# Kernel optimization log

Measured on AMD Instinct MI355X. Metric: run time of the kernel, lower is better.

The kernel has to match this reference:

```python
import jax, jax.numpy as jnp
import numpy as np

D_MODEL = 512
D_FF = 2048
VOCAB = 32000
B, N = 2, 384
EPS = 1e-6


def positional_encoding(n, d):
    pos = np.arange(n)[:, None].astype(np.float64)
    i = np.arange(d)[None, :]
    ang = pos / np.power(10000.0, (2 * (i // 2)) / np.float32(d))
    ang[:, 0::2] = np.sin(ang[:, 0::2])
    ang[:, 1::2] = np.cos(ang[:, 1::2])
    return jnp.asarray(ang, dtype=jnp.float32)  # [n, d]


def layer_norm(x, gamma, beta):
    mu = jnp.mean(x, axis=-1, keepdims=True)
    var = jnp.mean(jnp.square(x - mu), axis=-1, keepdims=True)
    return (x - mu) / jnp.sqrt(var + EPS) * gamma + beta


def setup_inputs() -> dict:
    key = jax.random.key(0)
    ks = jax.random.split(key, 12)
    s = 0.02
    return {
        "tokens": jax.random.randint(ks[0], (B, N), 0, VOCAB, dtype=jnp.int32),
        "emb": jax.random.normal(ks[1], (VOCAB, D_MODEL), jnp.float32) * s,
        "Wq": jax.random.normal(ks[2], (D_MODEL, D_MODEL), jnp.float32) * s,
        "bq": jnp.zeros((D_MODEL,), jnp.float32),
        "Wk": jax.random.normal(ks[3], (D_MODEL, D_MODEL), jnp.float32) * s,
        "bk": jnp.zeros((D_MODEL,), jnp.float32),
        "Wv": jax.random.normal(ks[4], (D_MODEL, D_MODEL), jnp.float32) * s,
        "bv": jnp.zeros((D_MODEL,), jnp.float32),
        "attn_scale": jax.random.normal(ks[5], (D_MODEL,), jnp.float32) * 0.05,
        "Wo": jax.random.normal(ks[6], (D_MODEL, D_MODEL), jnp.float32) * s,
        "bo": jnp.zeros((D_MODEL,), jnp.float32),
        "g1": jnp.ones((D_MODEL,), jnp.float32),
        "beta1": jnp.zeros((D_MODEL,), jnp.float32),
        "W1": jax.random.normal(ks[7], (D_MODEL, D_FF), jnp.float32) * s,
        "bf1": jnp.zeros((D_FF,), jnp.float32),
        "W2": jax.random.normal(ks[8], (D_FF, D_MODEL), jnp.float32) * s,
        "bf2": jnp.zeros((D_MODEL,), jnp.float32),
        "g2": jnp.ones((D_MODEL,), jnp.float32),
        "beta2": jnp.zeros((D_MODEL,), jnp.float32),
    }


def reference(tokens, emb, Wq, bq, Wk, bk, Wv, bv, attn_scale, Wo, bo,
              g1, beta1, W1, bf1, W2, bf2, g2, beta2):
    # Embedding + scaled positional encoding
    x = emb[tokens] * jnp.sqrt(jnp.float32(D_MODEL))  # [B, N, D]
    x = x + positional_encoding(N, D_MODEL)[None, :, :]

    # Additive (Bahdanau) self-attention
    q = x @ Wq + bq
    k = x @ Wk + bk  # note: original swaps key/value Dense layers; math-equivalent
    v = x @ Wv + bv
    # scores[b,i,j] = sum_d scale[d] * tanh(q[b,i,d] + k[b,j,d])  -> [B,N,N]
    scores = jnp.einsum("d,bijd->bij", attn_scale,
                        jnp.tanh(q[:, :, None, :] + k[:, None, :, :]))
    weights = jax.nn.softmax(scores, axis=-1)
    attn = jnp.einsum("bij,bjd->bid", weights, v)
    attn = attn @ Wo + bo
    x = layer_norm(x + attn, g1, beta1)

    # Feedforward + residual + LayerNorm
    h = jax.nn.relu(x @ W1 + bf1)
    y = h @ W2 + bf2
    return layer_norm(x + y, g2, beta2)
```

## Files before the change

kernel.cpp:

```cpp
#include <hip/hip_runtime.h>
#include <hip/hip_bf16.h>
#include <math.h>

#define D_MODEL 512
#define D_FF    2048
#define NBATCH  2
#define NSEQ    384
#define NROWS   (NBATCH * NSEQ)
#define LN_EPS  1e-6f

typedef __attribute__((ext_vector_type(8))) short short8;
typedef __attribute__((ext_vector_type(4))) short short4v;
typedef __attribute__((ext_vector_type(4))) float f32x4;
typedef __hip_bfloat16 bf16;

static __device__ __forceinline__ short bfb(float x) {
    bf16 h = __float2bfloat16(x);
    return *reinterpret_cast<short*>(&h);
}

__global__ __launch_bounds__(256) void wt_all_kernel(
    const float* __restrict__ Wq, const float* __restrict__ Wk,
    const float* __restrict__ Wv, const float* __restrict__ Wo,
    const float* __restrict__ W1, const float* __restrict__ W2,
    bf16* __restrict__ wqt, bf16* __restrict__ wkt, bf16* __restrict__ wvt,
    bf16* __restrict__ wot, bf16* __restrict__ w1t, bf16* __restrict__ w2t)
{
    int t = blockIdx.x;
    const float* W; bf16* Wt; int K, N, bx, by;
    if (t < 1024) {
        int w = t >> 8, rem = t & 255;
        W  = (w == 0) ? Wq  : (w == 1) ? Wk  : (w == 2) ? Wv  : Wo;
        Wt = (w == 0) ? wqt : (w == 1) ? wkt : (w == 2) ? wvt : wot;
        K = 512; N = 512; bx = rem & 15; by = rem >> 4;
    } else if (t < 2048) {
        int rem = t - 1024;
        W = W1; Wt = w1t; K = 512; N = 2048; bx = rem & 63; by = rem >> 6;
    } else {
        int rem = t - 2048;
        W = W2; Wt = w2t; K = 2048; N = 512; bx = rem & 15; by = rem >> 4;
    }

    __shared__ float tile[32][33];
    int tx = threadIdx.x & 31, ty = threadIdx.x >> 5;
    #pragma unroll
    for (int r = ty; r < 32; r += 8)
        tile[r][tx] = W[(size_t)(by * 32 + r) * N + bx * 32 + tx];
    __syncthreads();
    #pragma unroll
    for (int r = ty; r < 32; r += 8)
        Wt[(size_t)(bx * 32 + r) * K + by * 32 + tx] = __float2bfloat16(tile[tx][r]);
}

__global__ __launch_bounds__(256) void embed_pe_kernel(
    const int* __restrict__ tokens, const float* __restrict__ emb,
    float* __restrict__ x, bf16* __restrict__ xb)
{
    int row = blockIdx.x;
    int n   = row % NSEQ;
    int tok = tokens[row];
    const float sqrtD = 22.627416997969522f;
    for (int d = threadIdx.x; d < D_MODEL; d += 256) {
        float e = emb[tok * D_MODEL + d] * sqrtD;
        int   i2   = d & ~1;
        float expo = (float)i2 / (float)D_MODEL;
        float ang  = (float)n * powf(10000.0f, -expo);
        float pe   = (d & 1) ? cosf(ang) : sinf(ang);
        float val  = e + pe;
        x [(size_t)row * D_MODEL + d] = val;
        xb[(size_t)row * D_MODEL + d] = __float2bfloat16(val);
    }
}

__global__ __launch_bounds__(256) void qkv_mfma_kernel(
    const bf16* __restrict__ A,
    const bf16* __restrict__ wqt, const bf16* __restrict__ wkt, const bf16* __restrict__ wvt,
    const float* __restrict__ bq, const float* __restrict__ bk, const float* __restrict__ bv,
    float* __restrict__ aexp, float* __restrict__ bexp, bf16* __restrict__ vT)
{
    int z = blockIdx.z;
    const bf16*  Wt   = (z == 0) ? wqt : (z == 1) ? wkt : wvt;
    const float* bias = (z == 0) ? bq  : (z == 1) ? bk  : bv;

    int lane = threadIdx.x & 63, wid = threadIdx.x >> 6;
    int rowBase = blockIdx.y * 32 + (wid >> 1) * 16;
    int colBase = blockIdx.x * 64 + (wid & 1) * 32;

    const bf16* Ap  = A  + (size_t)(rowBase + (lane & 15)) * D_MODEL + ((lane >> 4) << 3);
    const bf16* Bp0 = Wt + (size_t)(colBase + (lane & 15)) * D_MODEL + ((lane >> 4) << 3);
    const bf16* Bp1 = Bp0 + (size_t)16 * D_MODEL;

    f32x4 acc0 = {0.f, 0.f, 0.f, 0.f};
    f32x4 acc1 = {0.f, 0.f, 0.f, 0.f};

    #pragma unroll 4
    for (int k0 = 0; k0 < D_MODEL; k0 += 32) {
        short8 a  = *reinterpret_cast<const short8*>(Ap  + k0);
        short8 b0 = *reinterpret_cast<const short8*>(Bp0 + k0);
        short8 b1 = *reinterpret_cast<const short8*>(Bp1 + k0);
        acc0 = __builtin_amdgcn_mfma_f32_16x16x32_bf16(a, b0, acc0, 0, 0, 0);
        acc1 = __builtin_amdgcn_mfma_f32_16x16x32_bf16(a, b1, acc1, 0, 0, 0);
    }

    int crow = rowBase + ((lane >> 4) << 2);
    int ccol = colBase + (lane & 15);

    if (z < 2) {
        float* C = (z == 0) ? aexp : bexp;
        #pragma unroll
        for (int r = 0; r < 4; ++r) {
            int row = crow + r;
            #pragma unroll
            for (int j = 0; j < 2; ++j) {
                int col = ccol + j * 16;
                float val = (j == 0 ? acc0[r] : acc1[r]) + bias[col];
                C[(size_t)row * D_MODEL + col] = __expf(2.0f * val);
            }
        }
    } else {
        int bb = crow / NSEQ;
        int jr = crow - bb * NSEQ;
        #pragma unroll
        for (int j = 0; j < 2; ++j) {
            int col = ccol + j * 16;
            short4v pk;
            #pragma unroll
            for (int r = 0; r < 4; ++r)
                pk[r] = bfb((j == 0 ? acc0[r] : acc1[r]) + bias[col]);
            size_t idx = ((size_t)bb * D_MODEL + col) * NSEQ + jr;
            *reinterpret_cast<short4v*>((short*)vT + idx) = pk;
        }
    }
}

__global__ __launch_bounds__(512) void score_softmax_kernel(
    const float* __restrict__ aexp, const float* __restrict__ bexp,
    const float* __restrict__ scale, bf16* __restrict__ P)
{
    int row0 = blockIdx.x * 2;
    int b    = row0 / NSEQ;
    int tid  = threadIdx.x;
    int lane = tid & 63, wid = tid >> 6;

    __shared__ float a0s[D_MODEL], a1s[D_MODEL], s2s[D_MODEL];
    __shared__ float sc[2][NSEQ];
    __shared__ float red[8];

    a0s[tid] = aexp[(size_t)row0 * D_MODEL + tid];
    a1s[tid] = aexp[(size_t)(row0 + 1) * D_MODEL + tid];
    s2s[tid] = -2.0f * scale[tid];
    __syncthreads();

    float a0[8], a1[8], sv[8];
    #pragma unroll
    for (int u = 0; u < 8; ++u) {
        a0[u] = a0s[lane * 8 + u];
        a1[u] = a1s[lane * 8 + u];
        sv[u] = s2s[lane * 8 + u];
    }

    const float* kb = bexp + (size_t)b * NSEQ * D_MODEL + lane * 8;
    for (int j = wid; j < NSEQ; j += 8) {
        const float4* kp = (const float4*)(kb + (size_t)j * D_MODEL);
        float4 b0 = kp[0], b1 = kp[1];
        float bb[8] = {b0.x, b0.y, b0.z, b0.w, b1.x, b1.y, b1.z, b1.w};
        float t0 = 0.0f, t1 = 0.0f;
        #pragma unroll
        for (int u = 0; u < 8; ++u) {
            float r0 = __builtin_amdgcn_rcpf(fmaf(a0[u], bb[u], 1.0f));
            float r1 = __builtin_amdgcn_rcpf(fmaf(a1[u], bb[u], 1.0f));
            t0 = fmaf(sv[u], r0, t0);
            t1 = fmaf(sv[u], r1, t1);
        }
        #pragma unroll
        for (int off = 32; off; off >>= 1) {
            t0 += __shfl_xor(t0, off, 64);
            t1 += __shfl_xor(t1, off, 64);
        }
        if (lane == 0) { sc[0][j] = t0; sc[1][j] = t1; }
    }
    __syncthreads();

    #pragma unroll
    for (int r = 0; r < 2; ++r) {
        float e = (tid < NSEQ) ? __expf(sc[r][tid]) : 0.0f;
        float s = e;
        #pragma unroll
        for (int off = 32; off; off >>= 1) s += __shfl_xor(s, off, 64);
        if (lane == 0) red[wid] = s;
        __syncthreads();
        if (tid == 0) {
            float t = 0.0f;
            #pragma unroll
            for (int w = 0; w < 8; ++w) t += red[w];
            red[0] = t;
        }
        __syncthreads();
        float inv = 1.0f / red[0];
        if (tid < NSEQ)
            P[(size_t)(row0 + r) * NSEQ + tid] = __float2bfloat16(e * inv);
        __syncthreads();
    }
}

__global__ __launch_bounds__(256) void pv_mfma_kernel(
    const bf16* __restrict__ P, const bf16* __restrict__ vT,
    bf16* __restrict__ attnb)
{
    int z = blockIdx.z;
    int lane = threadIdx.x & 63, wid = threadIdx.x >> 6;
    int rowBase = blockIdx.y * 32 + (wid >> 1) * 16;
    int colBase = blockIdx.x * 64 + (wid & 1) * 32;

    const bf16* Ap  = P  + ((size_t)z * NSEQ + rowBase + (lane & 15)) * NSEQ + ((lane >> 4) << 3);
    const bf16* Bp0 = vT + ((size_t)z * D_MODEL + colBase + (lane & 15)) * NSEQ + ((lane >> 4) << 3);
    const bf16* Bp1 = Bp0 + (size_t)16 * NSEQ;

    f32x4 acc0 = {0.f, 0.f, 0.f, 0.f};
    f32x4 acc1 = {0.f, 0.f, 0.f, 0.f};

    #pragma unroll 4
    for (int k0 = 0; k0 < NSEQ; k0 += 32) {
        short8 a  = *reinterpret_cast<const short8*>(Ap  + k0);
        short8 b0 = *reinterpret_cast<const short8*>(Bp0 + k0);
        short8 b1 = *reinterpret_cast<const short8*>(Bp1 + k0);
        acc0 = __builtin_amdgcn_mfma_f32_16x16x32_bf16(a, b0, acc0, 0, 0, 0);
        acc1 = __builtin_amdgcn_mfma_f32_16x16x32_bf16(a, b1, acc1, 0, 0, 0);
    }

    int crow = rowBase + ((lane >> 4) << 2);
    int ccol = colBase + (lane & 15);
    #pragma unroll
    for (int r = 0; r < 4; ++r)
        #pragma unroll
        for (int j = 0; j < 2; ++j)
            attnb[((size_t)z * NSEQ + crow + r) * D_MODEL + ccol + j * 16] =
                __float2bfloat16(j == 0 ? acc0[r] : acc1[r]);
}

__global__ __launch_bounds__(256) void mfma_gemm_kernel(
    const bf16* __restrict__ A, const bf16* __restrict__ Wt,
    const float* __restrict__ bias, const float* __restrict__ resid,
    float* __restrict__ Cf, bf16* __restrict__ Cb,
    int K, int N, int relu)
{
    int lane = threadIdx.x & 63, wid = threadIdx.x >> 6;
    int rowBase = blockIdx.y * 32 + (wid >> 1) * 16;
    int colBase = blockIdx.x * 64 + (wid & 1) * 32;

    const bf16* Ap  = A  + (size_t)(rowBase + (lane & 15)) * K + ((lane >> 4) << 3);
    const bf16* Bp0 = Wt + (size_t)(colBase + (lane & 15)) * K + ((lane >> 4) << 3);
    const bf16* Bp1 = Bp0 + (size_t)16 * K;

    f32x4 acc0 = {0.f, 0.f, 0.f, 0.f};
    f32x4 acc1 = {0.f, 0.f, 0.f, 0.f};

    #pragma unroll 4
    for (int k0 = 0; k0 < K; k0 += 32) {
        short8 a  = *reinterpret_cast<const short8*>(Ap  + k0);
        short8 b0 = *reinterpret_cast<const short8*>(Bp0 + k0);
        short8 b1 = *reinterpret_cast<const short8*>(Bp1 + k0);
        acc0 = __builtin_amdgcn_mfma_f32_16x16x32_bf16(a, b0, acc0, 0, 0, 0);
        acc1 = __builtin_amdgcn_mfma_f32_16x16x32_bf16(a, b1, acc1, 0, 0, 0);
    }

    int crow = rowBase + ((lane >> 4) << 2);
    int ccol = colBase + (lane & 15);
    #pragma unroll
    for (int r = 0; r < 4; ++r) {
        int row = crow + r;
        #pragma unroll
        for (int j = 0; j < 2; ++j) {
            int col = ccol + j * 16;
            float val = (j == 0 ? acc0[r] : acc1[r]) + bias[col];
            if (resid) val += resid[(size_t)row * N + col];
            if (relu)  val = fmaxf(val, 0.0f);
            if (Cf) Cf[(size_t)row * N + col] = val;
            if (Cb) Cb[(size_t)row * N + col] = __float2bfloat16(val);
        }
    }
}

__global__ __launch_bounds__(256) void ln_kernel(
    const float* __restrict__ in, const float* __restrict__ gamma,
    const float* __restrict__ beta, float* __restrict__ out,
    bf16* __restrict__ outb)
{
    int row = blockIdx.x;
    int tid = threadIdx.x;
    int lane = tid & 63, wid = tid >> 6;
    __shared__ float red[4];

    float v0 = in[(size_t)row * D_MODEL + tid];
    float v1 = in[(size_t)row * D_MODEL + tid + 256];

    float s = v0 + v1;
    #pragma unroll
    for (int off = 32; off; off >>= 1) s += __shfl_xor(s, off, 64);
    if (lane == 0) red[wid] = s;
    __syncthreads();
    if (tid == 0) red[0] = red[0] + red[1] + red[2] + red[3];
    __syncthreads();
    float mu = red[0] * (1.0f / D_MODEL);
    __syncthreads();

    float d0 = v0 - mu, d1 = v1 - mu;
    float s2 = d0 * d0 + d1 * d1;
    #pragma unroll
    for (int off = 32; off; off >>= 1) s2 += __shfl_xor(s2, off, 64);
    if (lane == 0) red[wid] = s2;
    __syncthreads();
    if (tid == 0) red[0] = red[0] + red[1] + red[2] + red[3];
    __syncthreads();
    float var = red[0] * (1.0f / D_MODEL);
    float inv = rsqrtf(var + LN_EPS);

    float o0 = d0 * inv * gamma[tid] + beta[tid];
    float o1 = d1 * inv * gamma[tid + 256] + beta[tid + 256];
    out[(size_t)row * D_MODEL + tid]       = o0;
    out[(size_t)row * D_MODEL + tid + 256] = o1;
    if (outb) {
        outb[(size_t)row * D_MODEL + tid]       = __float2bfloat16(o0);
        outb[(size_t)row * D_MODEL + tid + 256] = __float2bfloat16(o1);
    }
}

extern "C" void kernel_launch(void* const* d_in, const int* in_sizes, int n_in,
                              void* d_out, int out_size, void* d_ws, size_t ws_size,
                              hipStream_t stream)
{
    const int*   tokens = (const int*)  d_in[0];
    const float* emb    = (const float*)d_in[1];
    const float* Wq     = (const float*)d_in[2];
    const float* bq     = (const float*)d_in[3];
    const float* Wk     = (const float*)d_in[4];
    const float* bk     = (const float*)d_in[5];
    const float* Wv     = (const float*)d_in[6];
    const float* bv     = (const float*)d_in[7];
    const float* ascale = (const float*)d_in[8];
    const float* Wo     = (const float*)d_in[9];
    const float* bo     = (const float*)d_in[10];
    const float* g1     = (const float*)d_in[11];
    const float* beta1  = (const float*)d_in[12];
    const float* W1     = (const float*)d_in[13];
    const float* bf1    = (const float*)d_in[14];
    const float* W2     = (const float*)d_in[15];
    const float* bf2    = (const float*)d_in[16];
    const float* g2     = (const float*)d_in[17];
    const float* beta2  = (const float*)d_in[18];

    float* out = (float*)d_out;
    float* ws  = (float*)d_ws;

    const size_t SZ = (size_t)NROWS * D_MODEL;

    float* x0   = ws;
    float* aexp = ws + 1 * SZ;
    float* bexp = ws + 2 * SZ;
    float* t1 = aexp;
    float* x1 = bexp;
    float* y  = x0;

    bf16* x0b   = (bf16*)(ws + 3 * SZ);
    bf16* attnb = x0b + SZ;
    bf16* x1b   = attnb + SZ;
    bf16* hb    = x1b + SZ;
    bf16* Pb    = hb + (size_t)NROWS * D_FF;
    bf16* vTb   = Pb + (size_t)NBATCH * NSEQ * NSEQ;
    bf16* wqt   = vTb + (size_t)NBATCH * D_MODEL * NSEQ;
    bf16* wkt   = wqt + (size_t)D_MODEL * D_MODEL;
    bf16* wvt   = wkt + (size_t)D_MODEL * D_MODEL;
    bf16* wot   = wvt + (size_t)D_MODEL * D_MODEL;
    bf16* w1t   = wot + (size_t)D_MODEL * D_MODEL;
    bf16* w2t   = w1t + (size_t)D_MODEL * D_FF;

    wt_all_kernel<<<3072, 256, 0, stream>>>(Wq, Wk, Wv, Wo, W1, W2,
                                            wqt, wkt, wvt, wot, w1t, w2t);

    embed_pe_kernel<<<NROWS, 256, 0, stream>>>(tokens, emb, x0, x0b);

    qkv_mfma_kernel<<<dim3(D_MODEL / 64, NROWS / 32, 3), 256, 0, stream>>>(
        x0b, wqt, wkt, wvt, bq, bk, bv, aexp, bexp, vTb);

    score_softmax_kernel<<<NROWS / 2, 512, 0, stream>>>(aexp, bexp, ascale, Pb);

    pv_mfma_kernel<<<dim3(D_MODEL / 64, NSEQ / 32, NBATCH), 256, 0, stream>>>(
        Pb, vTb, attnb);

    mfma_gemm_kernel<<<dim3(D_MODEL / 64, NROWS / 32), 256, 0, stream>>>(
        attnb, wot, bo, x0, t1, nullptr, D_MODEL, D_MODEL, 0);

    ln_kernel<<<NROWS, 256, 0, stream>>>(t1, g1, beta1, x1, x1b);

    mfma_gemm_kernel<<<dim3(D_FF / 64, NROWS / 32), 256, 0, stream>>>(
        x1b, w1t, bf1, nullptr, nullptr, hb, D_MODEL, D_FF, 1);

    mfma_gemm_kernel<<<dim3(D_MODEL / 64, NROWS / 32), 256, 0, stream>>>(
        hb, w2t, bf2, x1, y, nullptr, D_FF, D_MODEL, 0);

    ln_kernel<<<NROWS, 256, 0, stream>>>(y, g2, beta2, out, nullptr);
}
```

Measured before the change: 138.4 us.

## Split score kernel across halves and defer softmax normalization into PV epilogue

The score kernel now runs on a 2D grid with each block handling half the key positions, mapping lanes to (key, d-chunk) pairs and loading query/scale vectors directly from global memory instead of staging in shared memory. It writes unnormalized exponentials and per-half partial sums, and the PV GEMM divides by the combined sum in its epilogue. This aims to raise parallelism and remove the in-kernel softmax barriers. It adds a small partial-sum buffer and keeps the unnormalized exp values in bf16, with no max subtraction.

```diff
diff --git a/kernel.cpp b/kernel.cpp
--- a/kernel.cpp
+++ b/kernel.cpp
@@ -133,86 +133,102 @@
     }
 }
 
-__global__ __launch_bounds__(512) void score_softmax_kernel(
+__global__ __launch_bounds__(512) void score_kernel(
     const float* __restrict__ aexp, const float* __restrict__ bexp,
-    const float* __restrict__ scale, bf16* __restrict__ P)
-{
-    int row0 = blockIdx.x * 2;
+    const float* __restrict__ scale, bf16* __restrict__ E,
+    float* __restrict__ Sp)
+{
+    int ip   = blockIdx.x;
+    int half = blockIdx.y;
+    int row0 = ip * 2;
     int b    = row0 / NSEQ;
     int tid  = threadIdx.x;
     int lane = tid & 63, wid = tid >> 6;
-
-    __shared__ float a0s[D_MODEL], a1s[D_MODEL], s2s[D_MODEL];
-    __shared__ float sc[2][NSEQ];
-    __shared__ float red[8];
-
-    a0s[tid] = aexp[(size_t)row0 * D_MODEL + tid];
-    a1s[tid] = aexp[(size_t)(row0 + 1) * D_MODEL + tid];
-    s2s[tid] = -2.0f * scale[tid];
-    __syncthreads();
-
-    float a0[8], a1[8], sv[8];
-    #pragma unroll
-    for (int u = 0; u < 8; ++u) {
-        a0[u] = a0s[lane * 8 + u];
-        a1[u] = a1s[lane * 8 + u];
-        sv[u] = s2s[lane * 8 + u];
-    }
-
-    const float* kb = bexp + (size_t)b * NSEQ * D_MODEL + lane * 8;
-    for (int j = wid; j < NSEQ; j += 8) {
-        const float4* kp = (const float4*)(kb + (size_t)j * D_MODEL);
-        float4 b0 = kp[0], b1 = kp[1];
-        float bb[8] = {b0.x, b0.y, b0.z, b0.w, b1.x, b1.y, b1.z, b1.w};
-        float t0 = 0.0f, t1 = 0.0f;
-        #pragma unroll
-        for (int u = 0; u < 8; ++u) {
-            float r0 = __builtin_amdgcn_rcpf(fmaf(a0[u], bb[u], 1.0f));
-            float r1 = __builtin_amdgcn_rcpf(fmaf(a1[u], bb[u], 1.0f));
-            t0 = fmaf(sv[u], r0, t0);
-            t1 = fmaf(sv[u], r1, t1);
-        }
-        #pragma unroll
-        for (int off = 32; off; off >>= 1) {
+    int jj = lane & 7, dd = lane >> 3;
+
+    const float* a0p = aexp + (size_t)row0 * D_MODEL;
+    const float* a1p = a0p + D_MODEL;
+    const float* bb  = bexp + (size_t)b * NSEQ * D_MODEL;
+
+    int jbase = half * 192 + wid * 8 + jj;
+
+    float acc[3][2] = {};
+
+    #pragma unroll
+    for (int chunk = 0; chunk < 8; ++chunk) {
+        int doff = chunk * 64 + dd * 8;
+        float4 a0A = *(const float4*)(a0p + doff);
+        float4 a0B = *(const float4*)(a0p + doff + 4);
+        float4 a1A = *(const float4*)(a1p + doff);
+        float4 a1B = *(const float4*)(a1p + doff + 4);
+        float4 sA  = *(const float4*)(scale + doff);
+        float4 sB  = *(const float4*)(scale + doff + 4);
+        float a0[8] = {a0A.x,a0A.y,a0A.z,a0A.w,a0B.x,a0B.y,a0B.z,a0B.w};
+        float a1[8] = {a1A.x,a1A.y,a1A.z,a1A.w,a1B.x,a1B.y,a1B.z,a1B.w};
+        float sv[8] = {sA.x,sA.y,sA.z,sA.w,sB.x,sB.y,sB.z,sB.w};
+
+        #pragma unroll
+        for (int o = 0; o < 3; ++o) {
+            const float* bp = bb + (size_t)(jbase + o * 64) * D_MODEL + doff;
+            float4 b0 = *(const float4*)(bp);
+            float4 b1 = *(const float4*)(bp + 4);
+            float bv8[8] = {b0.x,b0.y,b0.z,b0.w,b1.x,b1.y,b1.z,b1.w};
+            float t0 = acc[o][0], t1 = acc[o][1];
+            #pragma unroll
+            for (int u = 0; u < 8; ++u) {
+                float r0 = __builtin_amdgcn_rcpf(fmaf(a0[u], bv8[u], 1.0f));
+                float r1 = __builtin_amdgcn_rcpf(fmaf(a1[u], bv8[u], 1.0f));
+                t0 = fmaf(sv[u], r0, t0);
+                t1 = fmaf(sv[u], r1, t1);
+            }
+            acc[o][0] = t0; acc[o][1] = t1;
+        }
+    }
+
+    __shared__ float sred[8][2];
+    float es0 = 0.0f, es1 = 0.0f;
+    #pragma unroll
+    for (int o = 0; o < 3; ++o) {
+        int j = jbase + o * 64;
+        float t0 = acc[o][0], t1 = acc[o][1];
+        #pragma unroll
+        for (int off = 8; off < 64; off <<= 1) {
             t0 += __shfl_xor(t0, off, 64);
             t1 += __shfl_xor(t1, off, 64);
         }
-        if (lane == 0) { sc[0][j] = t0; sc[1][j] = t1; }
-    }
-    __syncthreads();
-
-    #pragma unroll
-    for (int r = 0; r < 2; ++r) {
-        float e = (tid < NSEQ) ? __expf(sc[r][tid]) : 0.0f;
-        float s = e;
-        #pragma unroll
-        for (int off = 32; off; off >>= 1) s += __shfl_xor(s, off, 64);
-        if (lane == 0) red[wid] = s;
-        __syncthreads();
-        if (tid == 0) {
-            float t = 0.0f;
-            #pragma unroll
-            for (int w = 0; w < 8; ++w) t += red[w];
-            red[0] = t;
-        }
-        __syncthreads();
-        float inv = 1.0f / red[0];
-        if (tid < NSEQ)
-            P[(size_t)(row0 + r) * NSEQ + tid] = __float2bfloat16(e * inv);
-        __syncthreads();
+        float e0 = __expf(-2.0f * t0);
+        float e1 = __expf(-2.0f * t1);
+        if (dd == 0) {
+            E[(size_t)row0 * NSEQ + j]       = __float2bfloat16(e0);
+            E[(size_t)(row0+1) * NSEQ + j]   = __float2bfloat16(e1);
+        }
+        es0 += e0; es1 += e1;
+    }
+    #pragma unroll
+    for (int off = 1; off < 64; off <<= 1) {
+        es0 += __shfl_xor(es0, off, 64);
+        es1 += __shfl_xor(es1, off, 64);
+    }
+    if (lane == 0) { sred[wid][0] = es0 * 0.125f; sred[wid][1] = es1 * 0.125f; }
+    __syncthreads();
+    if (tid < 2) {
+        float s = 0.0f;
+        #pragma unroll
+        for (int w = 0; w < 8; ++w) s += sred[w][tid];
+        Sp[(size_t)(row0 + tid) * 2 + half] = s;
     }
 }
 
 __global__ __launch_bounds__(256) void pv_mfma_kernel(
-    const bf16* __restrict__ P, const bf16* __restrict__ vT,
-    bf16* __restrict__ attnb)
+    const bf16* __restrict__ E, const bf16* __restrict__ vT,
+    const float* __restrict__ Sp, bf16* __restrict__ attnb)
 {
     int z = blockIdx.z;
     int lane = threadIdx.x & 63, wid = threadIdx.x >> 6;
     int rowBase = blockIdx.y * 32 + (wid >> 1) * 16;
     int colBase = blockIdx.x * 64 + (wid & 1) * 32;
 
-    const bf16* Ap  = P  + ((size_t)z * NSEQ + rowBase + (lane & 15)) * NSEQ + ((lane >> 4) << 3);
+    const bf16* Ap  = E  + ((size_t)z * NSEQ + rowBase + (lane & 15)) * NSEQ + ((lane >> 4) << 3);
     const bf16* Bp0 = vT + ((size_t)z * D_MODEL + colBase + (lane & 15)) * NSEQ + ((lane >> 4) << 3);
     const bf16* Bp1 = Bp0 + (size_t)16 * NSEQ;
 
@@ -231,11 +247,14 @@
     int crow = rowBase + ((lane >> 4) << 2);
     int ccol = colBase + (lane & 15);
     #pragma unroll
-    for (int r = 0; r < 4; ++r)
+    for (int r = 0; r < 4; ++r) {
+        int grow = z * NSEQ + crow + r;
+        float Sinv = 1.0f / (Sp[(size_t)grow * 2] + Sp[(size_t)grow * 2 + 1]);
         #pragma unroll
         for (int j = 0; j < 2; ++j)
-            attnb[((size_t)z * NSEQ + crow + r) * D_MODEL + ccol + j * 16] =
-                __float2bfloat16(j == 0 ? acc0[r] : acc1[r]);
+            attnb[(size_t)grow * D_MODEL + ccol + j * 16] =
+                __float2bfloat16((j == 0 ? acc0[r] : acc1[r]) * Sinv);
+    }
 }
 
 __global__ __launch_bounds__(256) void mfma_gemm_kernel(
@@ -365,14 +384,15 @@
     bf16* attnb = x0b + SZ;
     bf16* x1b   = attnb + SZ;
     bf16* hb    = x1b + SZ;
-    bf16* Pb    = hb + (size_t)NROWS * D_FF;
-    bf16* vTb   = Pb + (size_t)NBATCH * NSEQ * NSEQ;
+    bf16* Eb    = hb + (size_t)NROWS * D_FF;
+    bf16* vTb   = Eb + (size_t)NBATCH * NSEQ * NSEQ;
     bf16* wqt   = vTb + (size_t)NBATCH * D_MODEL * NSEQ;
     bf16* wkt   = wqt + (size_t)D_MODEL * D_MODEL;
     bf16* wvt   = wkt + (size_t)D_MODEL * D_MODEL;
     bf16* wot   = wvt + (size_t)D_MODEL * D_MODEL;
     bf16* w1t   = wot + (size_t)D_MODEL * D_MODEL;
     bf16* w2t   = w1t + (size_t)D_MODEL * D_FF;
+    float* Sp   = (float*)(w2t + (size_t)D_FF * D_MODEL);
 
     wt_all_kernel<<<3072, 256, 0, stream>>>(Wq, Wk, Wv, Wo, W1, W2,
                                             wqt, wkt, wvt, wot, w1t, w2t);
@@ -382,10 +402,10 @@
     qkv_mfma_kernel<<<dim3(D_MODEL / 64, NROWS / 32, 3), 256, 0, stream>>>(
         x0b, wqt, wkt, wvt, bq, bk, bv, aexp, bexp, vTb);
 
-    score_softmax_kernel<<<NROWS / 2, 512, 0, stream>>>(aexp, bexp, ascale, Pb);
+    score_kernel<<<dim3(NROWS / 2, 2), 512, 0, stream>>>(aexp, bexp, ascale, Eb, Sp);
 
     pv_mfma_kernel<<<dim3(D_MODEL / 64, NSEQ / 32, NBATCH), 256, 0, stream>>>(
-        Pb, vTb, attnb);
+        Eb, vTb, Sp, attnb);
 
     mfma_gemm_kernel<<<dim3(D_MODEL / 64, NROWS / 32), 256, 0, stream>>>(
         attnb, wot, bo, x0, t1, nullptr, D_MODEL, D_MODEL, 0);
```

Result: slower. 187.4 us (+35.4%).
